# Performance work log

Hardware: AMD Instinct MI355X
Metric: run time of the kernel (lower is better)

The kernel has to match this reference:

```python
import jax, jax.numpy as jnp
import numpy as np

NEG_INF = -1e9


def setup_inputs() -> dict:
    key = jax.random.key(0)
    ks = jax.random.split(key, 12)
    B, Tq, Tki, E, D, M = 4, 2048, 2048, 1024, 128, 16384
    return {
        "x": jax.random.normal(ks[0], (B, Tq, E), jnp.float32),
        "ki": jax.random.normal(ks[1], (B, Tki, E), jnp.float32),
        "vi": jax.random.normal(ks[2], (B, Tki, E), jnp.float32),
        "mem_keys": jax.random.normal(ks[3], (B, M, D), jnp.float32),
        "mem_vals": jax.random.normal(ks[4], (B, M, D), jnp.float32),
        "Wq": jax.random.normal(ks[5], (E, D), jnp.float32) / np.sqrt(E),
        "bq": jax.random.normal(ks[6], (D,), jnp.float32) * 0.02,
        "Wk": jax.random.normal(ks[7], (E, D), jnp.float32) / np.sqrt(E),
        "bk": jax.random.normal(ks[8], (D,), jnp.float32) * 0.02,
        "Wv": jax.random.normal(ks[9], (E, D), jnp.float32) / np.sqrt(E),
        "bv": jax.random.normal(ks[10], (D,), jnp.float32) * 0.02,
        "gate": jax.random.normal(ks[11], (1,), jnp.float32),
        "idx": 3,
    }


def reference(x, ki, vi, mem_keys, mem_vals, Wq, bq, Wk, bk, Wv, bv, gate, idx):
    B, Tq, E = x.shape
    D = Wq.shape[1]
    top_k = 32
    q = x @ Wq + bq            # [B,Tq,D]
    k = x @ Wk + bk            # [B,Tq,D]
    v = x @ Wv + bv
    s = idx * D                # idx is a python int -> static slice
    k_full = jnp.concatenate([ki[:, :, s:s + D], k], axis=1)   # [B,Tk,D]
    v_full = jnp.concatenate([vi[:, :, s:s + D], v], axis=1)
    Tk = k_full.shape[1]
    # causal SDPA over prefix+current, offset diagonal Tk-Tq
    scores = jnp.einsum("bqd,bkd->bqk", q, k_full) / jnp.sqrt(jnp.float32(D))
    i = jnp.arange(Tq)[:, None]
    j = jnp.arange(Tk)[None, :]
    causal = j <= i + (Tk - Tq)
    scores = jnp.where(causal, scores, NEG_INF)
    att = jax.nn.softmax(scores, axis=-1)
    out = jnp.einsum("bqk,bkd->bqd", att, v_full)              # [B,Tq,D]
    # kNN memory attention: exact top-k inner-product search per query
    mem_scores = jnp.einsum("btd,bmd->btm", q, mem_keys)       # [B,Tq,M]
    _, top_idx = jax.lax.top_k(mem_scores, top_k)              # [B,Tq,K]
    gather = jax.vmap(lambda mem, ix: mem[ix])                 # per batch
    mem_k = gather(mem_keys, top_idx)                          # [B,Tq,K,D]
    mem_v = gather(mem_vals, top_idx)
    # note: original scales by sqrt(Cq)=sqrt(n_embd), not sqrt(head_size)
    mem_att = jax.nn.softmax(
        jnp.einsum("btd,btkd->btk", q, mem_k) / jnp.sqrt(jnp.float32(E)), axis=-1)
    mem_out = jnp.einsum("btk,btkd->btd", mem_att, mem_v)      # [B,Tq,D]
    md_out = out * gate + mem_out * (1.0 - gate)
    return md_out
```

## Files before the change

kernel.cpp:

```cpp
#include <hip/hip_runtime.h>


using bf16x8 = __attribute__((ext_vector_type(8))) short;
using f32x4  = __attribute__((ext_vector_type(4))) float;

typedef __attribute__((address_space(1))) const void GVoid;
typedef __attribute__((address_space(3))) void LVoid;
__device__ __forceinline__ void gl16(const ushort* g, ushort* l) {
  __builtin_amdgcn_global_load_lds((GVoid*)g, (LVoid*)l, 16, 0, 0);
}

__device__ __forceinline__ float bf2f(ushort h) {
  union { uint u; float f; } x; x.u = ((uint)h) << 16; return x.f;
}
__device__ __forceinline__ ushort f2bf(float f) {
  union { float f; uint u; } x; x.f = f;
  uint u = x.u;
  u += 0x7fffu + ((u >> 16) & 1u);
  return (ushort)(u >> 16);
}
__device__ __forceinline__ uint ord2(uint v) {
  uint lo = v & 0xffffu, hi = v >> 16;
  lo = (lo & 0x8000u) ? (0xffffu ^ lo) : (lo | 0x8000u);
  hi = (hi & 0x8000u) ? (0xffffu ^ hi) : (hi | 0x8000u);
  return lo | (hi << 16);
}

__global__ __launch_bounds__(256) void k_wt(const float* __restrict__ Wq,
                                            const float* __restrict__ Wk,
                                            const float* __restrict__ Wv,
                                            ushort* __restrict__ Wth,
                                            ushort* __restrict__ Wtlq) {
  int id = blockIdx.x * 256 + threadIdx.x;
  int z = id >> 17, r = id & 131071;
  int n = r >> 10, k = r & 1023;
  const float* W = (z == 1) ? Wk : (z == 2) ? Wv : Wq;
  float w = W[k * 128 + n];
  ushort h = f2bf(w);
  if (z < 3) Wth[id] = h;
  else       Wtlq[r] = f2bf(w - bf2f(h));
}

__global__ __launch_bounds__(256) void k_cvt8(const float* __restrict__ src,
                                              ushort* __restrict__ dst) {
  int id = blockIdx.x * 256 + threadIdx.x;
  size_t base = (size_t)id * 8;
  float4 a = *(const float4*)(src + base);
  float4 b = *(const float4*)(src + base + 4);
  bf16x8 r;
  r[0] = (short)f2bf(a.x); r[1] = (short)f2bf(a.y);
  r[2] = (short)f2bf(a.z); r[3] = (short)f2bf(a.w);
  r[4] = (short)f2bf(b.x); r[5] = (short)f2bf(b.y);
  r[6] = (short)f2bf(b.z); r[7] = (short)f2bf(b.w);
  *(bf16x8*)(dst + base) = r;
}

__global__ __launch_bounds__(256) void k_xsplit(const float* __restrict__ x,
                                                ushort* __restrict__ xh,
                                                ushort* __restrict__ xl) {
  int id = blockIdx.x * 256 + threadIdx.x;
  size_t base = (size_t)id * 8;
  float4 a = *(const float4*)(x + base);
  float4 b = *(const float4*)(x + base + 4);
  float xf[8] = {a.x, a.y, a.z, a.w, b.x, b.y, b.z, b.w};
  bf16x8 rh, rl;
#pragma unroll
  for (int j = 0; j < 8; ++j) {
    ushort h = f2bf(xf[j]);
    rh[j] = (short)h;
    rl[j] = (short)f2bf(xf[j] - bf2f(h));
  }
  *(bf16x8*)(xh + base) = rh;
  *(bf16x8*)(xl + base) = rl;
}

__global__ __launch_bounds__(256) void k_prefix(const float* __restrict__ ki,
                                                const float* __restrict__ vi,
                                                const int* __restrict__ idx,
                                                ushort* __restrict__ kfull,
                                                ushort* __restrict__ vfull) {
  int s = idx[0] * 128;
  int id = blockIdx.x * 256 + threadIdx.x;
  int d8 = (id & 15) * 8;
  int bt = id >> 4;
  int b = bt >> 11, t = bt & 2047;
  const float* kp = ki + (size_t)bt * 1024 + s + d8;
  const float* vp = vi + (size_t)bt * 1024 + s + d8;
  bf16x8 rk, rv;
#pragma unroll
  for (int j = 0; j < 8; ++j) { rk[j] = (short)f2bf(kp[j]); rv[j] = (short)f2bf(vp[j]); }
  size_t dst = ((size_t)b * 4096 + t) * 128 + d8;
  *(bf16x8*)(kfull + dst) = rk;
  *(bf16x8*)(vfull + dst) = rv;
}

__global__ __launch_bounds__(256) void k_qkv3(const ushort* __restrict__ xh,
                                              const ushort* __restrict__ xl,
                                              const ushort* __restrict__ Wth,
                                              const ushort* __restrict__ Wtlq,
                                              const float* __restrict__ bq,
                                              const float* __restrict__ bk,
                                              const float* __restrict__ bv,
                                              float* __restrict__ qex,
                                              ushort* __restrict__ kfull,
                                              ushort* __restrict__ vfull) {
  __shared__ ushort lds[2][16384];
  int z = blockIdx.z;
  int g = blockIdx.y;
  int m0 = blockIdx.x * 64;
  int tid = threadIdx.x;
  int w = tid >> 6, lane = tid & 63;
  int l15 = lane & 15, q8 = (lane >> 4) * 8;
  const ushort* Wz = Wth + (size_t)z * 131072;
  const ushort* xh_src = xh + (size_t)(m0 + w * 16 + l15) * 1024 + q8;
  const ushort* xl_src = xl + (size_t)(m0 + w * 16 + l15) * 1024 + q8;
  const ushort* wh_src = Wz   + (size_t)(g * 64 + w * 16 + l15) * 1024 + q8;
  const ushort* wl_src = Wtlq + (size_t)(g * 64 + w * 16 + l15) * 1024 + q8;
  int sb = w * 1024;

  f32x4 zero = {0.f, 0.f, 0.f, 0.f};
  f32x4 acc[4] = {zero, zero, zero, zero};

  {
    ushort* B = &lds[0][0];
    gl16(xh_src,      B + sb);
    gl16(xh_src + 32, B + sb + 512);
    gl16(wh_src,      B + 8192 + sb);
    gl16(wh_src + 32, B + 8192 + sb + 512);
    if (z == 0) {
      gl16(xl_src,      B + 4096 + sb);
      gl16(xl_src + 32, B + 4096 + sb + 512);
      gl16(wl_src,      B + 12288 + sb);
      gl16(wl_src + 32, B + 12288 + sb + 512);
    }
  }
  __syncthreads();
  int bf = 0;
  for (int t16 = 0; t16 < 16; ++t16) {
    if (t16 < 15) {
      int k0 = t16 * 64 + 64;
      ushort* B = &lds[bf ^ 1][0];
      gl16(xh_src + k0,      B + sb);
      gl16(xh_src + k0 + 32, B + sb + 512);
      gl16(wh_src + k0,      B + 8192 + sb);
      gl16(wh_src + k0 + 32, B + 8192 + sb + 512);
      if (z == 0) {
        gl16(xl_src + k0,      B + 4096 + sb);
        gl16(xl_src + k0 + 32, B + 4096 + sb + 512);
        gl16(wl_src + k0,      B + 12288 + sb);
        gl16(wl_src + k0 + 32, B + 12288 + sb + 512);
      }
    }
    const ushort* B = &lds[bf][0];
    int lo = lane * 8;
    if (z == 0) {
#pragma unroll
      for (int kc = 0; kc < 2; ++kc) {
        bf16x8 ah = *(const bf16x8*)(B + (w * 2 + kc) * 512 + lo);
        bf16x8 al = *(const bf16x8*)(B + 4096 + (w * 2 + kc) * 512 + lo);
#pragma unroll
        for (int cc = 0; cc < 4; ++cc) {
          bf16x8 bh = *(const bf16x8*)(B + 8192 + (cc * 2 + kc) * 512 + lo);
          bf16x8 bl = *(const bf16x8*)(B + 12288 + (cc * 2 + kc) * 512 + lo);
          acc[cc] = __builtin_amdgcn_mfma_f32_16x16x32_bf16(ah, bh, acc[cc], 0, 0, 0);
          acc[cc] = __builtin_amdgcn_mfma_f32_16x16x32_bf16(ah, bl, acc[cc], 0, 0, 0);
          acc[cc] = __builtin_amdgcn_mfma_f32_16x16x32_bf16(al, bh, acc[cc], 0, 0, 0);
        }
      }
    } else {
#pragma unroll
      for (int kc = 0; kc < 2; ++kc) {
        bf16x8 ah = *(const bf16x8*)(B + (w * 2 + kc) * 512 + lo);
#pragma unroll
        for (int cc = 0; cc < 4; ++cc) {
          bf16x8 bh = *(const bf16x8*)(B + 8192 + (cc * 2 + kc) * 512 + lo);
          acc[cc] = __builtin_amdgcn_mfma_f32_16x16x32_bf16(ah, bh, acc[cc], 0, 0, 0);
        }
      }
    }
    __syncthreads();
    bf ^= 1;
  }

  const float* bias = (z == 0) ? bq : (z == 1) ? bk : bv;
  int mrow = m0 + w * 16 + (lane >> 4) * 4;
#pragma unroll
  for (int cc = 0; cc < 4; ++cc) {
    int n = g * 64 + cc * 16 + l15;
    float bb = bias[n];
#pragma unroll
    for (int r = 0; r < 4; ++r) {
      int m = mrow + r;
      float val = acc[cc][r] + bb;
      if (z == 0) {
        qex[(size_t)m * 128 + n] = val;
      } else {
        int b2 = m >> 11, tt = m & 2047;
        size_t o = ((size_t)b2 * 4096 + 2048 + tt) * 128 + n;
        if (z == 1) kfull[o] = f2bf(val); else vfull[o] = f2bf(val);
      }
    }
  }
}

__global__ __launch_bounds__(256) void k_vt(const ushort* __restrict__ vfull,
                                            ushort* __restrict__ Vt) {
  __shared__ ushort lds[64][136];
  int blk = blockIdx.x;
  int b = blk >> 6, t0 = (blk & 63) * 64;
  int t = threadIdx.x;
#pragma unroll
  for (int p = 0; p < 4; ++p) {
    int ch = p * 256 + t;
    int row = ch >> 4, c8 = (ch & 15) * 8;
    uint4 v = *(const uint4*)(vfull + ((size_t)b * 4096 + t0 + row) * 128 + c8);
    *(uint4*)(&lds[row][c8]) = v;
  }
  __syncthreads();
#pragma unroll
  for (int p = 0; p < 8; ++p) {
    int q = p * 256 + t;
    int d = q >> 4, t4 = (q & 15) * 4;
    ushort4 o;
    o.x = lds[t4 + 0][d]; o.y = lds[t4 + 1][d];
    o.z = lds[t4 + 2][d]; o.w = lds[t4 + 3][d];
    *(ushort4*)(Vt + ((size_t)b * 128 + d) * 4096 + t0 + t4) = o;
  }
}

__global__ __launch_bounds__(256) void k_scores(const float* __restrict__ A,
                                                const ushort* __restrict__ Bm,
                                                ushort* __restrict__ S,
                                                int N, int nslice, int causalOff,
                                                long sA, long sB, long sS) {
  __shared__ ushort Bt[64 * 136];
  int q0 = blockIdx.x * 64;
  int ns0 = blockIdx.y * nslice;
  int nend = ns0 + nslice; if (nend > N) nend = N;
  int climit = q0 + 64 + causalOff; if (nend > climit) nend = climit;
  if (ns0 >= nend) return;
  int zb = blockIdx.z;
  const float*  Ab = A  + (size_t)zb * sA;
  const ushort* Bb = Bm + (size_t)zb * sB;
  ushort* Sb = S + (size_t)zb * sS;
  int t = threadIdx.x, lane = t & 63, wv = t >> 6;
  int l15 = lane & 15, q8 = (lane >> 4) * 8;
  const float* Arow = Ab + (size_t)(q0 + wv * 16 + l15) * 128 + q8;
  bf16x8 af[4];
#pragma unroll
  for (int kc = 0; kc < 4; ++kc)
#pragma unroll
    for (int j = 0; j < 8; ++j) af[kc][j] = (short)f2bf(Arow[kc * 32 + j]);
  for (int n0 = ns0; n0 < nend; n0 += 64) {
#pragma unroll
    for (int p = 0; p < 4; ++p) {
      int ch = p * 256 + t;
      int row = ch >> 4, c8 = (ch & 15) * 8;
      uint4 v = *(const uint4*)(Bb + (size_t)(n0 + row) * 128 + c8);
      *(uint4*)(&Bt[row * 136 + c8]) = v;
    }
    __syncthreads();
    f32x4 zero = {0.f, 0.f, 0.f, 0.f};
    f32x4 acc[4] = {zero, zero, zero, zero};
#pragma unroll
    for (int h = 0; h < 4; ++h) {
#pragma unroll
      for (int kc = 0; kc < 4; ++kc) {
        bf16x8 bfr = *(const bf16x8*)(&Bt[(h * 16 + l15) * 136 + kc * 32 + q8]);
        acc[h] = __builtin_amdgcn_mfma_f32_16x16x32_bf16(af[kc], bfr, acc[h], 0, 0, 0);
      }
    }
    int qq = q0 + wv * 16 + (lane >> 4) * 4;
#pragma unroll
    for (int h = 0; h < 4; ++h)
#pragma unroll
      for (int r = 0; r < 4; ++r)
        Sb[(size_t)(qq + r) * N + (n0 + h * 16 + l15)] = f2bf(acc[h][r]);
    __syncthreads();
  }
}

__global__ __launch_bounds__(256) void k_softmax(ushort* __restrict__ S) {
  int rid = blockIdx.x;
  int i = rid & 2047;
  ushort* row = S + (size_t)rid * 4096;
  int w = i + 2049;
  int t = threadIdx.x;
  const float scale = 0.08838834764831845f;
  float v[16];
  float mx = -1e30f;
#pragma unroll
  for (int c = 0; c < 16; ++c) {
    int e = c * 256 + t;
    float f = -1e30f;
    if (e < w) f = bf2f(row[e]) * scale;
    v[c] = f;
    mx = fmaxf(mx, f);
  }
  __shared__ float red[4];
#pragma unroll
  for (int off = 32; off; off >>= 1) mx = fmaxf(mx, __shfl_xor(mx, off));
  if ((t & 63) == 0) red[t >> 6] = mx;
  __syncthreads();
  mx = fmaxf(fmaxf(red[0], red[1]), fmaxf(red[2], red[3]));
  __syncthreads();
  float ex[16];
  float sum = 0.f;
#pragma unroll
  for (int c = 0; c < 16; ++c) {
    int e = c * 256 + t;
    ex[c] = (e < w) ? __expf(v[c] - mx) : 0.f;
    sum += ex[c];
  }
#pragma unroll
  for (int off = 32; off; off >>= 1) sum += __shfl_xor(sum, off);
  if ((t & 63) == 0) red[t >> 6] = sum;
  __syncthreads();
  sum = red[0] + red[1] + red[2] + red[3];
  float inv = 1.f / sum;
#pragma unroll
  for (int c = 0; c < 16; ++c) {
    int e = c * 256 + t;
    row[e] = f2bf(ex[c] * inv);
  }
}

__global__ __launch_bounds__(128) void k_pv(const ushort* __restrict__ P,
                                            const ushort* __restrict__ Vt,
                                            float* __restrict__ O) {
  int b = blockIdx.z;
  int d0 = blockIdx.y * 64;
  int q0 = blockIdx.x * 32;
  int t = threadIdx.x, lane = t & 63, wv = t >> 6;
  int l15 = lane & 15, q8 = (lane >> 4) * 8;
  const ushort* Pb = P + ((size_t)b * 2048 + q0 + wv * 16 + l15) * 4096;
  const ushort* Vb = Vt + (size_t)b * 128 * 4096;
  int kend = q0 + 32 + 2048; if (kend > 4096) kend = 4096;
  f32x4 zero = {0.f, 0.f, 0.f, 0.f};
  f32x4 acc[4] = {zero, zero, zero, zero};
  for (int k0 = 0; k0 < kend; k0 += 32) {
    bf16x8 af = *(const bf16x8*)(Pb + k0 + q8);
#pragma unroll
    for (int nc = 0; nc < 4; ++nc) {
      bf16x8 bfr = *(const bf16x8*)(Vb + (size_t)(d0 + nc * 16 + l15) * 4096 + k0 + q8);
      acc[nc] = __builtin_amdgcn_mfma_f32_16x16x32_bf16(af, bfr, acc[nc], 0, 0, 0);
    }
  }
  size_t ob = ((size_t)b * 2048 + q0 + wv * 16 + (lane >> 4) * 4) * 128;
#pragma unroll
  for (int nc = 0; nc < 4; ++nc)
#pragma unroll
    for (int r = 0; r < 4; ++r)
      O[ob + (size_t)r * 128 + d0 + nc * 16 + l15] = acc[nc][r];
}

__global__ __launch_bounds__(256) void k_topk(const ushort* __restrict__ Sall,
                                              const float* __restrict__ qf32b,
                                              const float* __restrict__ memk,
                                              const float* __restrict__ memv,
                                              float* __restrict__ mout) {
  __shared__ uint sred[32];
  __shared__ float qf[128];
  __shared__ uint cidx[384];
  __shared__ float csc[384];
  __shared__ unsigned long long ckey[384];
  __shared__ uint selIdx[32];
  __shared__ float selS[32];
  __shared__ float obuf[256];
  __shared__ int nC;

  int i = blockIdx.x;
  const ushort* Srow = Sall + (size_t)i * 16384;
  int t = threadIdx.x;
  int wv = t >> 6, lane = t & 63;
  if (t < 128) qf[t] = qf32b[(size_t)i * 128 + t];
  if (t == 0) nC = 0;

  uint keys[32];
#pragma unroll
  for (int c = 0; c < 8; ++c) {
    int base = (c * 256 + t) * 8;
    uint4 rv = *(const uint4*)(Srow + base);
    keys[c * 4 + 0] = ord2(rv.x);
    keys[c * 4 + 1] = ord2(rv.y);
    keys[c * 4 + 2] = ord2(rv.z);
    keys[c * 4 + 3] = ord2(rv.w);
  }
  uint mymax = 0;
#pragma unroll
  for (int r = 0; r < 32; ++r) {
    uint v = keys[r];
    uint hi = v >> 16, lo = v & 0xffffu;
    uint mm = hi > lo ? hi : lo;
    mymax = mm > mymax ? mm : mymax;
  }
#pragma unroll
  for (int off = 32; off; off >>= 1) {
    uint o = __shfl_xor(mymax, off);
    mymax = o > mymax ? o : mymax;
  }
  if (lane == 0) sred[wv] = mymax;
  __syncthreads();
  uint M = sred[0];
  { uint a = sred[1]; M = a > M ? a : M;
    a = sred[2]; M = a > M ? a : M;
    a = sred[3]; M = a > M ? a : M; }
  __syncthreads();

  uint T;
  uint MbCur = M >> 5;
  uint carry = 0;
  while (true) {
    uint h0 = 0, h1 = 0;
#pragma unroll
    for (int r = 0; r < 32; ++r) {
      uint v = keys[r];
      uint blo = MbCur - ((v & 0xffffu) >> 5);
      uint bhi = MbCur - (v >> 21);
      if (blo < 8u) { uint a = 1u << ((blo & 3u) << 3); if (blo < 4u) h0 += a; else h1 += a; }
      if (bhi < 8u) { uint a = 1u << ((bhi & 3u) << 3); if (bhi < 4u) h0 += a; else h1 += a; }
    }
    uint c8[8] = {h0 & 255u, (h0 >> 8) & 255u, (h0 >> 16) & 255u, h0 >> 24,
                  h1 & 255u, (h1 >> 8) & 255u, (h1 >> 16) & 255u, h1 >> 24};
#pragma unroll
    for (int b = 0; b < 8; ++b)
#pragma unroll
      for (int off = 32; off; off >>= 1) c8[b] += __shfl_xor(c8[b], off);
    if (lane == 0) {
#pragma unroll
      for (int b = 0; b < 8; ++b) sred[wv * 8 + b] = c8[b];
    }
    __syncthreads();
    uint cum = carry; int bstar = -1;
#pragma unroll
    for (int b = 0; b < 8; ++b) {
      uint tb = sred[b] + sred[8 + b] + sred[16 + b] + sred[24 + b];
      cum += tb;
      if (bstar < 0 && cum >= 64u) bstar = b;
    }
    if (bstar >= 0) { T = (MbCur - (uint)bstar) << 5; break; }
    carry = cum;
    MbCur -= 8u;
    __syncthreads();
  }

#pragma unroll
  for (int r = 0; r < 32; ++r) {
    uint v = keys[r];
    int base = ((r >> 2) * 256 + t) * 8 + ((r & 3) * 2);
    if ((v & 0xffffu) >= T) { int p = atomicAdd(&nC, 1); if (p < 384) cidx[p] = (uint)base; }
    if ((v >> 16) >= T)     { int p = atomicAdd(&nC, 1); if (p < 384) cidx[p] = (uint)(base + 1); }
  }
  __syncthreads();
  int C = nC; if (C > 384) C = 384;
  {
    float qa = qf[lane * 2], qb = qf[lane * 2 + 1];
    for (int j0 = wv; j0 < C; j0 += 32) {
      float2 pp[8];
      float s[8];
#pragma unroll
      for (int u = 0; u < 8; ++u) {
        int j = j0 + u * 4;
        if (j < C) pp[u] = *(const float2*)(memk + (size_t)cidx[j] * 128 + lane * 2);
      }
#pragma unroll
      for (int u = 0; u < 8; ++u) {
        int j = j0 + u * 4;
        s[u] = (j < C) ? (qa * pp[u].x + qb * pp[u].y) : 0.f;
      }
#pragma unroll
      for (int off = 32; off; off >>= 1) {
#pragma unroll
        for (int u = 0; u < 8; ++u) s[u] += __shfl_xor(s[u], off);
      }
      if (lane == 0) {
#pragma unroll
        for (int u = 0; u < 8; ++u) {
          int j = j0 + u * 4;
          if (j < C) csc[j] = s[u];
        }
      }
    }
  }
  __syncthreads();
  for (int j = t; j < C; j += 256) {
    uint sb2 = __float_as_uint(csc[j]);
    uint o = (sb2 & 0x80000000u) ? ~sb2 : (sb2 | 0x80000000u);
    ckey[j] = ((unsigned long long)o << 32) | (uint)(~cidx[j]);
  }
  __syncthreads();
  for (int j = t; j < C; j += 256) {
    unsigned long long my = ckey[j];
    int rank = 0;
    for (int l = 0; l < C; ++l) rank += (ckey[l] > my) ? 1 : 0;
    if (rank < 32) { selS[rank] = csc[j]; selIdx[rank] = cidx[j]; }
  }
  __syncthreads();
  if (wv == 0) {
    float sc = (lane < 32) ? selS[lane] * 0.03125f : -1e30f;
    float mx = sc;
#pragma unroll
    for (int off = 32; off; off >>= 1) mx = fmaxf(mx, __shfl_xor(mx, off));
    float ex = (lane < 32) ? __expf(sc - mx) : 0.f;
    float Z = ex;
#pragma unroll
    for (int off = 32; off; off >>= 1) Z += __shfl_xor(Z, off);
    if (lane < 32) selS[lane] = ex / Z;
  }
  __syncthreads();
  {
    int d = t & 127, half = t >> 7;
    float vv[16];
#pragma unroll
    for (int u = 0; u < 16; ++u)
      vv[u] = memv[(size_t)selIdx[half * 16 + u] * 128 + d];
    float acc = 0.f;
#pragma unroll
    for (int u = 0; u < 16; ++u)
      acc += selS[half * 16 + u] * vv[u];
    obuf[t] = acc;
  }
  __syncthreads();
  if (t < 128) mout[(size_t)i * 128 + t] = obuf[t] + obuf[t + 128];
}

__global__ __launch_bounds__(256) void k_mix(const float* __restrict__ a,
                                             const float* __restrict__ b,
                                             const float* __restrict__ gate,
                                             float* __restrict__ out) {
  int id = blockIdx.x * 256 + threadIdx.x;
  float g = gate[0];
  float4 va = ((const float4*)a)[id];
  float4 vb = ((const float4*)b)[id];
  float4 o;
  o.x = va.x * g + vb.x * (1.f - g);
  o.y = va.y * g + vb.y * (1.f - g);
  o.z = va.z * g + vb.z * (1.f - g);
  o.w = va.w * g + vb.w * (1.f - g);
  ((float4*)out)[id] = o;
}

extern "C" void kernel_launch(void* const* d_in, const int* in_sizes, int n_in,
                              void* d_out, int out_size, void* d_ws, size_t ws_size,
                              hipStream_t stream) {
  const float* x    = (const float*)d_in[0];
  const float* ki   = (const float*)d_in[1];
  const float* vi   = (const float*)d_in[2];
  const float* mk   = (const float*)d_in[3];
  const float* mv   = (const float*)d_in[4];
  const float* Wq   = (const float*)d_in[5];
  const float* bq   = (const float*)d_in[6];
  const float* Wk   = (const float*)d_in[7];
  const float* bk   = (const float*)d_in[8];
  const float* Wv   = (const float*)d_in[9];
  const float* bv   = (const float*)d_in[10];
  const float* gate = (const float*)d_in[11];
  const int*   idx  = (const int*)d_in[12];

  char* ws = (char*)d_ws;
  ushort* Sbuf  = (ushort*)(ws);
  ushort* xh    = (ushort*)(ws);
  ushort* xl    = (ushort*)(ws + 16777216);
  float*  qex   = (float*) (ws + 67108864);
  ushort* kfull = (ushort*)(ws + 71303168);
  ushort* vfull = (ushort*)(ws + 75497472);
  ushort* Vt    = (ushort*)(ws + 79691776);
  ushort* mkb   = (ushort*)(ws + 83886080);
  ushort* Wth   = (ushort*)(ws + 100663296);
  ushort* Wtlq  = (ushort*)(ws + 101449728);
  float*  osdpa = (float*) (ws + 101711872);
  float*  mout  = (float*) (ws + 105906176);

  k_wt<<<2048, 256, 0, stream>>>(Wq, Wk, Wv, Wth, Wtlq);
  k_cvt8<<<4096, 256, 0, stream>>>(mk, mkb);
  k_xsplit<<<4096, 256, 0, stream>>>(x, xh, xl);
  k_prefix<<<512, 256, 0, stream>>>(ki, vi, idx, kfull, vfull);

  k_qkv3<<<dim3(128, 2, 3), 256, 0, stream>>>(xh, xl, Wth, Wtlq, bq, bk, bv,
                                              qex, kfull, vfull);
  k_vt<<<256, 256, 0, stream>>>(vfull, Vt);

  k_scores<<<dim3(32, 4, 4), 256, 0, stream>>>(qex, kfull, Sbuf,
                                               4096, 1024, 2048,
                                               (long)2048 * 128, (long)4096 * 128,
                                               (long)2048 * 4096);
  k_softmax<<<8192, 256, 0, stream>>>(Sbuf);
  k_pv<<<dim3(64, 2, 4), 128, 0, stream>>>(Sbuf, Vt, osdpa);

  for (int b = 0; b < 4; ++b) {
    k_scores<<<dim3(32, 8, 1), 256, 0, stream>>>(qex + (size_t)b * 2048 * 128,
                                                 mkb + (size_t)b * 16384 * 128,
                                                 Sbuf, 16384, 2048, (1 << 28),
                                                 0, 0, 0);
    k_topk<<<2048, 256, 0, stream>>>(Sbuf, qex + (size_t)b * 2048 * 128,
                                     mk + (size_t)b * 16384 * 128,
                                     mv + (size_t)b * 16384 * 128,
                                     mout + (size_t)b * 2048 * 128);
  }

  k_mix<<<1024, 256, 0, stream>>>(osdpa, mout, gate, (float*)d_out);
}
```

Baseline: 735.4 us.

## Double-buffer P and V tiles through LDS in the PV kernel

The PV matmul kernel used to load P and V fragments straight from global memory into registers on every 32-wide k step. It now stages 64-wide k tiles of P and V into a two-slot LDS buffer with async global_load_lds, prefetching the next tile while MFMAs run on the current one. Each wave loads a share of the V tile, so V is fetched once per block instead of by every wave. This adds LDS use and a barrier on each k step.

New measurement: 710.3 us. -3.4%, faster.

```diff
diff --git a/kernel.cpp b/kernel.cpp
--- a/kernel.cpp
+++ b/kernel.cpp
@@ -328,25 +328,61 @@
 __global__ __launch_bounds__(128) void k_pv(const ushort* __restrict__ P,
                                             const ushort* __restrict__ Vt,
                                             float* __restrict__ O) {
+  __shared__ ushort lds[2][6144];
   int b = blockIdx.z;
   int d0 = blockIdx.y * 64;
   int q0 = blockIdx.x * 32;
-  int t = threadIdx.x, lane = t & 63, wv = t >> 6;
+  int t = threadIdx.x, lane = t & 63, w = t >> 6;
   int l15 = lane & 15, q8 = (lane >> 4) * 8;
-  const ushort* Pb = P + ((size_t)b * 2048 + q0 + wv * 16 + l15) * 4096;
+  const ushort* Pq = P + ((size_t)b * 2048 + q0) * 4096;
   const ushort* Vb = Vt + (size_t)b * 128 * 4096;
+  const ushort* p_src  = Pq + (size_t)(w * 16 + l15) * 4096 + q8;
+  const ushort* v_src0 = Vb + (size_t)(d0 + (w * 2 + 0) * 16 + l15) * 4096 + q8;
+  const ushort* v_src1 = Vb + (size_t)(d0 + (w * 2 + 1) * 16 + l15) * 4096 + q8;
   int kend = q0 + 32 + 2048; if (kend > 4096) kend = 4096;
+  int ksteps = (kend + 63) >> 6;
+
   f32x4 zero = {0.f, 0.f, 0.f, 0.f};
   f32x4 acc[4] = {zero, zero, zero, zero};
-  for (int k0 = 0; k0 < kend; k0 += 32) {
-    bf16x8 af = *(const bf16x8*)(Pb + k0 + q8);
-#pragma unroll
-    for (int nc = 0; nc < 4; ++nc) {
-      bf16x8 bfr = *(const bf16x8*)(Vb + (size_t)(d0 + nc * 16 + l15) * 4096 + k0 + q8);
-      acc[nc] = __builtin_amdgcn_mfma_f32_16x16x32_bf16(af, bfr, acc[nc], 0, 0, 0);
-    }
-  }
-  size_t ob = ((size_t)b * 2048 + q0 + wv * 16 + (lane >> 4) * 4) * 128;
+
+  {
+    ushort* B = &lds[0][0];
+    gl16(p_src,       B + (w * 2 + 0) * 512);
+    gl16(p_src + 32,  B + (w * 2 + 1) * 512);
+    gl16(v_src0,      B + 2048 + ((w * 2 + 0) * 2 + 0) * 512);
+    gl16(v_src0 + 32, B + 2048 + ((w * 2 + 0) * 2 + 1) * 512);
+    gl16(v_src1,      B + 2048 + ((w * 2 + 1) * 2 + 0) * 512);
+    gl16(v_src1 + 32, B + 2048 + ((w * 2 + 1) * 2 + 1) * 512);
+  }
+  __syncthreads();
+  int bf = 0;
+  for (int st = 0; st < ksteps; ++st) {
+    if (st + 1 < ksteps) {
+      int k0 = st * 64 + 64;
+      ushort* B = &lds[bf ^ 1][0];
+      gl16(p_src + k0,       B + (w * 2 + 0) * 512);
+      gl16(p_src + k0 + 32,  B + (w * 2 + 1) * 512);
+      gl16(v_src0 + k0,      B + 2048 + ((w * 2 + 0) * 2 + 0) * 512);
+      gl16(v_src0 + k0 + 32, B + 2048 + ((w * 2 + 0) * 2 + 1) * 512);
+      gl16(v_src1 + k0,      B + 2048 + ((w * 2 + 1) * 2 + 0) * 512);
+      gl16(v_src1 + k0 + 32, B + 2048 + ((w * 2 + 1) * 2 + 1) * 512);
+    }
+    const ushort* B = &lds[bf][0];
+    int lo = lane * 8;
+#pragma unroll
+    for (int kc = 0; kc < 2; ++kc) {
+      bf16x8 af = *(const bf16x8*)(B + (w * 2 + kc) * 512 + lo);
+#pragma unroll
+      for (int nc = 0; nc < 4; ++nc) {
+        bf16x8 bfr = *(const bf16x8*)(B + 2048 + (nc * 2 + kc) * 512 + lo);
+        acc[nc] = __builtin_amdgcn_mfma_f32_16x16x32_bf16(af, bfr, acc[nc], 0, 0, 0);
+      }
+    }
+    __syncthreads();
+    bf ^= 1;
+  }
+
+  size_t ob = ((size_t)b * 2048 + q0 + w * 16 + (lane >> 4) * 4) * 128;
 #pragma unroll
   for (int nc = 0; nc < 4; ++nc)
 #pragma unroll
```
